# Kernel optimization log

Hardware: AMD Instinct MI355X
Metric: run time of the kernel (lower is better)

The kernel has to match this reference:

```python
import jax, jax.numpy as jnp
import numpy as np

B, D, Q = 1024, 512, 32768


def setup_inputs() -> dict:
    key = jax.random.key(0)
    kx, kq = jax.random.split(key)
    x = jax.random.normal(kx, (B, D), dtype=jnp.float32)
    queue_prev = jax.random.normal(kq, (Q, D), dtype=jnp.float32)
    return {"x": x, "queue_prev": queue_prev}


def reference(x, queue_prev):
    # Queue.forward: enqueue x, keep last queue_size rows (queue assumed full)
    q_size = queue_prev.shape[0]
    queue = jnp.concatenate([queue_prev, x], axis=0)[-q_size:]  # [Q, D]

    # euclidean metric == torch.cdist(x, queue): [B, Q]
    d2 = (
        jnp.sum(x * x, axis=-1, keepdims=True)
        + jnp.sum(queue * queue, axis=-1)[None, :]
        - 2.0 * (x @ queue.T)
    )
    dist = jnp.sqrt(jnp.maximum(d2, 0.0))

    # topk(-dist, 2): two smallest distances; take the 2nd (skip self-match)
    _, indices = jax.lax.top_k(-dist, 2)  # [B, 2]
    nn_idx = indices[:, -1]  # [B]
    return queue[nn_idx]  # [B, D]
```

## Files before the change

kernel.cpp:

```cpp
#include <hip/hip_runtime.h>
#include <hip/hip_bf16.h>
#include <hip/hip_fp16.h>

#define B_N 1024
#define D_N 512
#define Q_N 32768
#define QSHIFT (Q_N - B_N)

#define KP 1024
#define KL 1536
#define BKx 32
#define NKB (KL / BKx)
#define NCH 256

typedef __attribute__((ext_vector_type(8))) _Float16 half8;
typedef __attribute__((ext_vector_type(4))) float f32x4;

__device__ __forceinline__ void top2_update(float d, int j,
                                            float& d1, int& i1, float& d2, int& i2) {
  if (d < d1 || (d == d1 && j < i1)) { d2 = d1; i2 = i1; d1 = d; i1 = j; }
  else if (d < d2 || (d == d2 && j < i2)) { d2 = d; i2 = j; }
}

__global__ __launch_bounds__(256) void prep_kernel(const float* __restrict__ x,
                                                   const float* __restrict__ qp,
                                                   _Float16* __restrict__ Qpk,
                                                   _Float16* __restrict__ Apk,
                                                   float* __restrict__ q2n) {
  const int row  = blockIdx.x * 4 + (threadIdx.x >> 6);
  const int lane = threadIdx.x & 63;
  const bool is_q = row < Q_N;
  const float* src;
  _Float16* dst;
  if (is_q) {
    src = (row < QSHIFT) ? qp + (size_t)(row + B_N) * D_N
                         : x  + (size_t)(row - QSHIFT) * D_N;
    dst = Qpk + (size_t)row * KP;
  } else {
    src = x + (size_t)(row - Q_N) * D_N;
    dst = Apk + (size_t)(row - Q_N) * KP;
  }
  const float4* p = (const float4*)src;
  float4 a = p[lane * 2], b = p[lane * 2 + 1];
  float v[8] = {a.x, a.y, a.z, a.w, b.x, b.y, b.z, b.w};
  _Float16 hi[8] __attribute__((aligned(16)));
  _Float16 lo[8] __attribute__((aligned(16)));
  float s = 0.0f;
  #pragma unroll
  for (int u = 0; u < 8; ++u) {
    s += v[u] * v[u];
    hi[u] = (_Float16)v[u];
    lo[u] = (_Float16)(v[u] - (float)hi[u]);
  }
  *(uint4*)(dst + lane * 8)       = *(const uint4*)hi;
  *(uint4*)(dst + 512 + lane * 8) = *(const uint4*)lo;
  if (is_q) {
    #pragma unroll
    for (int off = 32; off; off >>= 1) s += __shfl_down(s, off);
    if (lane == 0) q2n[row] = s;
  }
}

__global__ __launch_bounds__(256) void nn_mfma(const _Float16* __restrict__ Apk,
                                               const _Float16* __restrict__ Qpk,
                                               const float* __restrict__ q2n,
                                               float4* __restrict__ partial) {
  __shared__ __align__(128) char smem[16384];

  const int chunk = blockIdx.x;
  const int mblk  = blockIdx.y;
  const int n0 = chunk * 128;
  const int i0 = mblk * 128;
  const int t = threadIdx.x;
  const int lane = t & 63;
  const int wv = t >> 6;
  const int wm = (wv >> 1) * 64;
  const int wn = (wv & 1) * 64;
  const int srow = lane >> 2;
  const int scol = (lane & 3) * 8;
  const int fr = lane & 15;
  const int fg = lane >> 4;
  const int fk = fg * 8;

  f32x4 acc[4][4] = {};

  for (int kb = 0; kb < NKB; ++kb) {
    int ka, kq;
    if (kb < 16)      { ka = kb * 32;              kq = kb * 32; }
    else if (kb < 32) { ka = 512 + (kb - 16) * 32; kq = (kb - 16) * 32; }
    else              { ka = (kb - 32) * 32;       kq = 512 + (kb - 32) * 32; }

    __syncthreads();
    #pragma unroll
    for (int c = 0; c < 2; ++c) {
      const int r = c * 64 + wv * 16;
      const _Float16* ga = Apk + (size_t)(i0 + r + srow) * KP + ka + scol;
      const _Float16* gb = Qpk + (size_t)(n0 + r + srow) * KP + kq + scol;
      __builtin_amdgcn_global_load_lds(
          (const __attribute__((address_space(1))) void*)ga,
          (__attribute__((address_space(3))) void*)(smem + r * 64), 16, 0, 0);
      __builtin_amdgcn_global_load_lds(
          (const __attribute__((address_space(1))) void*)gb,
          (__attribute__((address_space(3))) void*)(smem + 8192 + r * 64), 16, 0, 0);
    }
    asm volatile("s_waitcnt vmcnt(0)" ::: "memory");
    __syncthreads();

    half8 af[4], bf[4];
    #pragma unroll
    for (int mi = 0; mi < 4; ++mi)
      af[mi] = *(const half8*)(smem + ((wm + mi * 16 + fr) * 32 + fk) * 2);
    #pragma unroll
    for (int ni = 0; ni < 4; ++ni)
      bf[ni] = *(const half8*)(smem + 8192 + ((wn + ni * 16 + fr) * 32 + fk) * 2);
    #pragma unroll
    for (int mi = 0; mi < 4; ++mi)
      #pragma unroll
      for (int ni = 0; ni < 4; ++ni)
        acc[mi][ni] = __builtin_amdgcn_mfma_f32_16x16x32_f16(af[mi], bf[ni], acc[mi][ni], 0, 0, 0);
  }

  __syncthreads();
  float4 (*red)[8] = (float4(*)[8])smem;

  float q2v[4];
  #pragma unroll
  for (int ni = 0; ni < 4; ++ni) q2v[ni] = q2n[n0 + wn + ni * 16 + fr];

  #pragma unroll
  for (int mi = 0; mi < 4; ++mi) {
    #pragma unroll
    for (int r = 0; r < 4; ++r) {
      float d1 = 3.4e38f, d2v = 3.4e38f;
      int   i1 = 0x7fffffff, i2v = 0x7fffffff;
      #pragma unroll
      for (int ni = 0; ni < 4; ++ni) {
        const float d = q2v[ni] - 2.0f * acc[mi][ni][r];
        top2_update(d, n0 + wn + ni * 16 + fr, d1, i1, d2v, i2v);
      }
      #pragma unroll
      for (int off = 1; off <= 2; off <<= 1) {
        float e1 = __shfl_xor(d1, off);  int j1 = __shfl_xor(i1, off);
        float e2 = __shfl_xor(d2v, off); int j2 = __shfl_xor(i2v, off);
        top2_update(e1, j1, d1, i1, d2v, i2v);
        top2_update(e2, j2, d1, i1, d2v, i2v);
      }
      if ((lane & 3) == 0)
        red[wm + mi * 16 + fg * 4 + r][(wv & 1) * 4 + (fr >> 2)] =
            make_float4(d1, __int_as_float(i1), d2v, __int_as_float(i2v));
    }
  }
  __syncthreads();

  {
    const int row = t >> 1, part = t & 1;
    float d1 = 3.4e38f, d2 = 3.4e38f;
    int   i1 = 0x7fffffff, i2 = 0x7fffffff;
    #pragma unroll
    for (int u = 0; u < 4; ++u) {
      float4 v = red[row][part * 4 + u];
      top2_update(v.x, __float_as_int(v.y), d1, i1, d2, i2);
      top2_update(v.z, __float_as_int(v.w), d1, i1, d2, i2);
    }
    float e1 = __shfl_xor(d1, 1); int j1 = __shfl_xor(i1, 1);
    float e2 = __shfl_xor(d2, 1); int j2 = __shfl_xor(i2, 1);
    top2_update(e1, j1, d1, i1, d2, i2);
    top2_update(e2, j2, d1, i1, d2, i2);
    if (part == 0)
      partial[(size_t)(i0 + row) * NCH + chunk] =
          make_float4(d1, __int_as_float(i1), d2, __int_as_float(i2));
  }
}

__global__ __launch_bounds__(128) void nn_merge256(const float* __restrict__ x,
                                                   const float* __restrict__ qp,
                                                   const float4* __restrict__ partial,
                                                   float* __restrict__ out) {
  const int row = blockIdx.x;
  const int t   = threadIdx.x;
  __shared__ int s_nn;
  if (t < 64) {
    float d1 = 3.4e38f, d2 = 3.4e38f;
    int   i1 = 0x7fffffff, i2 = 0x7fffffff;
    #pragma unroll
    for (int u = 0; u < 4; ++u) {
      float4 v = partial[(size_t)row * NCH + u * 64 + t];
      top2_update(v.x, __float_as_int(v.y), d1, i1, d2, i2);
      top2_update(v.z, __float_as_int(v.w), d1, i1, d2, i2);
    }
    #pragma unroll
    for (int off = 1; off < 64; off <<= 1) {
      float e1 = __shfl_xor(d1, off); int j1 = __shfl_xor(i1, off);
      float e2 = __shfl_xor(d2, off); int j2 = __shfl_xor(i2, off);
      top2_update(e1, j1, d1, i1, d2, i2);
      top2_update(e2, j2, d1, i1, d2, i2);
    }
    if (t == 0) s_nn = i2;
  }
  __syncthreads();
  const int nn = s_nn;
  const float* src = (nn < QSHIFT) ? qp + (size_t)(nn + B_N) * D_N
                                   : x  + (size_t)(nn - QSHIFT) * D_N;
  ((float4*)(out + (size_t)row * D_N))[t] = ((const float4*)src)[t];
}

#define TM 64
#define TN 64
#define BKf 16
#define JCHUNK 512
#define NCHUNK (Q_N / JCHUNK)

__global__ __launch_bounds__(256) void qnorm_kernel(const float* __restrict__ x,
                                                    const float* __restrict__ qp,
                                                    float* __restrict__ q2) {
  const int row  = blockIdx.x * 4 + (threadIdx.x >> 6);
  const int lane = threadIdx.x & 63;
  const float* src = (row < QSHIFT) ? (qp + (size_t)(row + B_N) * D_N)
                                    : (x  + (size_t)(row - QSHIFT) * D_N);
  const float4* p = (const float4*)src;
  float4 a = p[lane];
  float4 b = p[lane + 64];
  float s = a.x*a.x + a.y*a.y + a.z*a.z + a.w*a.w
          + b.x*b.x + b.y*b.y + b.z*b.z + b.w*b.w;
  #pragma unroll
  for (int off = 32; off; off >>= 1) s += __shfl_down(s, off);
  if (lane == 0) q2[row] = s;
}

__global__ __launch_bounds__(256) void nn_main(const float* __restrict__ x,
                                               const float* __restrict__ qp,
                                               const float* __restrict__ q2,
                                               float4* __restrict__ partial) {
  __shared__ float As[BKf][TM];
  __shared__ float Bs[BKf][TN];
  __shared__ float4 red[TM][16];
  const int chunk = blockIdx.x;
  const int i0    = blockIdx.y * TM;
  const int t     = threadIdx.x;
  const int tx    = t & 15;
  const int ty    = t >> 4;
  const int lrow  = t >> 2;
  const int kp    = t & 3;
  float d1[4], d2v[4];
  int   i1[4], i2v[4];
  #pragma unroll
  for (int m = 0; m < 4; ++m) { d1[m] = 3.4e38f; d2v[m] = 3.4e38f; i1[m] = 0x7fffffff; i2v[m] = 0x7fffffff; }
  const int j_base = chunk * JCHUNK;
  for (int jt = 0; jt < JCHUNK / TN; ++jt) {
    const int j0 = j_base + jt * TN;
    float acc[4][4] = {};
    const int jr = j0 + lrow;
    const float* bsrc = (jr < QSHIFT) ? (qp + (size_t)(jr + B_N) * D_N)
                                      : (x  + (size_t)(jr - QSHIFT) * D_N);
    const float* asrc = x + (size_t)(i0 + lrow) * D_N;
    for (int k0 = 0; k0 < D_N; k0 += BKf) {
      float4 a4 = *(const float4*)&asrc[k0 + kp * 4];
      float4 b4 = *(const float4*)&bsrc[k0 + kp * 4];
      __syncthreads();
      As[kp*4+0][lrow] = a4.x; As[kp*4+1][lrow] = a4.y;
      As[kp*4+2][lrow] = a4.z; As[kp*4+3][lrow] = a4.w;
      Bs[kp*4+0][lrow] = b4.x; Bs[kp*4+1][lrow] = b4.y;
      Bs[kp*4+2][lrow] = b4.z; Bs[kp*4+3][lrow] = b4.w;
      __syncthreads();
      #pragma unroll
      for (int kk = 0; kk < BKf; ++kk) {
        float4 av = *(const float4*)&As[kk][ty * 4];
        float4 bv = *(const float4*)&Bs[kk][tx * 4];
        float am[4] = {av.x, av.y, av.z, av.w};
        float bm[4] = {bv.x, bv.y, bv.z, bv.w};
        #pragma unroll
        for (int m = 0; m < 4; ++m)
          #pragma unroll
          for (int c = 0; c < 4; ++c)
            acc[m][c] = fmaf(am[m], bm[c], acc[m][c]);
      }
    }
    #pragma unroll
    for (int m = 0; m < 4; ++m)
      #pragma unroll
      for (int c = 0; c < 4; ++c) {
        const int j = j0 + tx * 4 + c;
        const float d = q2[j] - 2.0f * acc[m][c];
        top2_update(d, j, d1[m], i1[m], d2v[m], i2v[m]);
      }
  }
  __syncthreads();
  #pragma unroll
  for (int m = 0; m < 4; ++m)
    red[ty * 4 + m][tx] = make_float4(d1[m], __int_as_float(i1[m]),
                                      d2v[m], __int_as_float(i2v[m]));
  __syncthreads();
  if (t < TM) {
    float bd1 = 3.4e38f, bd2 = 3.4e38f;
    int   bi1 = 0x7fffffff, bi2 = 0x7fffffff;
    #pragma unroll
    for (int u = 0; u < 16; ++u) {
      float4 v = red[t][u];
      top2_update(v.x, __float_as_int(v.y), bd1, bi1, bd2, bi2);
      top2_update(v.z, __float_as_int(v.w), bd1, bi1, bd2, bi2);
    }
    partial[(size_t)(i0 + t) * NCHUNK + chunk] =
        make_float4(bd1, __int_as_float(bi1), bd2, __int_as_float(bi2));
  }
}

__global__ __launch_bounds__(128) void nn_merge(const float* __restrict__ x,
                                                const float* __restrict__ qp,
                                                const float4* __restrict__ partial,
                                                float* __restrict__ out) {
  const int row = blockIdx.x;
  const int t   = threadIdx.x;
  __shared__ int s_nn;
  if (t < 64) {
    float4 v = partial[(size_t)row * NCHUNK + t];
    float d1 = v.x, d2 = v.z;
    int   i1 = __float_as_int(v.y), i2 = __float_as_int(v.w);
    #pragma unroll
    for (int off = 1; off < 64; off <<= 1) {
      float e1 = __shfl_xor(d1, off); int j1 = __shfl_xor(i1, off);
      float e2 = __shfl_xor(d2, off); int j2 = __shfl_xor(i2, off);
      top2_update(e1, j1, d1, i1, d2, i2);
      top2_update(e2, j2, d1, i1, d2, i2);
    }
    if (t == 0) s_nn = i2;
  }
  __syncthreads();
  const int nn = s_nn;
  const float* src = (nn < QSHIFT) ? (qp + (size_t)(nn + B_N) * D_N)
                                   : (x  + (size_t)(nn - QSHIFT) * D_N);
  *(float4*)&out[(size_t)row * D_N + t * 4] = *(const float4*)&src[t * 4];
}

extern "C" void kernel_launch(void* const* d_in, const int* in_sizes, int n_in,
                              void* d_out, int out_size, void* d_ws, size_t ws_size,
                              hipStream_t stream) {
  const float* x  = (const float*)d_in[0];
  const float* qp = (const float*)d_in[1];
  float* out = (float*)d_out;

  const size_t off_apk = 0;
  const size_t off_qpk = off_apk + (size_t)B_N * KP * sizeof(_Float16);
  const size_t off_q2n = off_qpk + (size_t)Q_N * KP * sizeof(_Float16);
  const size_t off_par = off_q2n + (size_t)Q_N * sizeof(float);
  const size_t need    = off_par + (size_t)B_N * NCH * sizeof(float4);

  if (ws_size >= need) {
    _Float16* Apk = (_Float16*)((char*)d_ws + off_apk);
    _Float16* Qpk = (_Float16*)((char*)d_ws + off_qpk);
    float*    q2n = (float*)((char*)d_ws + off_q2n);
    float4*   par = (float4*)((char*)d_ws + off_par);
    prep_kernel<<<(Q_N + B_N) / 4, 256, 0, stream>>>(x, qp, Qpk, Apk, q2n);
    nn_mfma<<<dim3(NCH, B_N / 128), 256, 0, stream>>>(Apk, Qpk, q2n, par);
    nn_merge256<<<B_N, 128, 0, stream>>>(x, qp, par, out);
  } else {
    float*  q2      = (float*)d_ws;
    float4* partial = (float4*)((char*)d_ws + Q_N * sizeof(float));
    qnorm_kernel<<<Q_N / 4, 256, 0, stream>>>(x, qp, q2);
    nn_main<<<dim3(NCHUNK, B_N / TM), 256, 0, stream>>>(x, qp, q2, partial);
    nn_merge<<<B_N, 128, 0, stream>>>(x, qp, partial, out);
  }
}
```

Measured before the change: 437.7 us.

## Double-buffer LDS tiles, swizzle LDS layout, and remap blocks for locality

```diff
diff --git a/kernel.cpp b/kernel.cpp
--- a/kernel.cpp
+++ b/kernel.cpp
@@ -61,66 +61,79 @@
   }
 }
 
-__global__ __launch_bounds__(256) void nn_mfma(const _Float16* __restrict__ Apk,
-                                               const _Float16* __restrict__ Qpk,
-                                               const float* __restrict__ q2n,
-                                               float4* __restrict__ partial) {
-  __shared__ __align__(128) char smem[16384];
-
-  const int chunk = blockIdx.x;
-  const int mblk  = blockIdx.y;
+__global__ __launch_bounds__(256, 3) void nn_mfma(const _Float16* __restrict__ Apk,
+                                                  const _Float16* __restrict__ Qpk,
+                                                  const float* __restrict__ q2n,
+                                                  float4* __restrict__ partial) {
+  __shared__ __align__(128) char smem[32768];
+
+  const int bid  = blockIdx.x;
+  const int work = (bid & 7) * 256 + (bid >> 3);
+  const int chunk = work >> 3;
+  const int mblk  = work & 7;
   const int n0 = chunk * 128;
   const int i0 = mblk * 128;
+
   const int t = threadIdx.x;
   const int lane = t & 63;
   const int wv = t >> 6;
   const int wm = (wv >> 1) * 64;
   const int wn = (wv & 1) * 64;
   const int srow = lane >> 2;
-  const int scol = (lane & 3) * 8;
+  const int gcol = (((lane & 3) ^ ((lane >> 3) & 3)) * 8);
   const int fr = lane & 15;
   const int fg = lane >> 4;
-  const int fk = fg * 8;
+  const int rswz = (fg ^ ((fr >> 1) & 3)) * 16;
 
   f32x4 acc[4][4] = {};
 
-  for (int kb = 0; kb < NKB; ++kb) {
+  auto stage = [&](int buf, int kb) {
     int ka, kq;
-    if (kb < 16)      { ka = kb * 32;              kq = kb * 32; }
+    if (kb < 16)      { ka = kb * 32;              kq = ka; }
     else if (kb < 32) { ka = 512 + (kb - 16) * 32; kq = (kb - 16) * 32; }
     else              { ka = (kb - 32) * 32;       kq = 512 + (kb - 32) * 32; }
-
-    __syncthreads();
+    char* base = smem + buf * 16384;
     #pragma unroll
     for (int c = 0; c < 2; ++c) {
       const int r = c * 64 + wv * 16;
-      const _Float16* ga = Apk + (size_t)(i0 + r + srow) * KP + ka + scol;
-      const _Float16* gb = Qpk + (size_t)(n0 + r + srow) * KP + kq + scol;
+      const _Float16* ga = Apk + (size_t)(i0 + r + srow) * KP + ka + gcol;
+      const _Float16* gb = Qpk + (size_t)(n0 + r + srow) * KP + kq + gcol;
       __builtin_amdgcn_global_load_lds(
           (const __attribute__((address_space(1))) void*)ga,
-          (__attribute__((address_space(3))) void*)(smem + r * 64), 16, 0, 0);
+          (__attribute__((address_space(3))) void*)(base + r * 64), 16, 0, 0);
       __builtin_amdgcn_global_load_lds(
           (const __attribute__((address_space(1))) void*)gb,
-          (__attribute__((address_space(3))) void*)(smem + 8192 + r * 64), 16, 0, 0);
-    }
+          (__attribute__((address_space(3))) void*)(base + 8192 + r * 64), 16, 0, 0);
+    }
+  };
+
+  stage(0, 0);
+  asm volatile("s_waitcnt vmcnt(0)" ::: "memory");
+  __syncthreads();
+
+  int cur = 0;
+  for (int kb = 0; kb < NKB; ++kb) {
+    if (kb + 1 < NKB) stage(cur ^ 1, kb + 1);
+
+    const char* base = smem + cur * 16384;
+    half8 af[4], bf[4];
+    #pragma unroll
+    for (int mi = 0; mi < 4; ++mi)
+      af[mi] = *(const half8*)(base + (wm + mi * 16 + fr) * 64 + rswz);
+    #pragma unroll
+    for (int ni = 0; ni < 4; ++ni)
+      bf[ni] = *(const half8*)(base + 8192 + (wn + ni * 16 + fr) * 64 + rswz);
+    #pragma unroll
+    for (int mi = 0; mi < 4; ++mi)
+      #pragma unroll
+      for (int ni = 0; ni < 4; ++ni)
+        acc[mi][ni] = __builtin_amdgcn_mfma_f32_16x16x32_f16(af[mi], bf[ni], acc[mi][ni], 0, 0, 0);
+
     asm volatile("s_waitcnt vmcnt(0)" ::: "memory");
     __syncthreads();
-
-    half8 af[4], bf[4];
-    #pragma unroll
-    for (int mi = 0; mi < 4; ++mi)
-      af[mi] = *(const half8*)(smem + ((wm + mi * 16 + fr) * 32 + fk) * 2);
-    #pragma unroll
-    for (int ni = 0; ni < 4; ++ni)
-      bf[ni] = *(const half8*)(smem + 8192 + ((wn + ni * 16 + fr) * 32 + fk) * 2);
-    #pragma unroll
-    for (int mi = 0; mi < 4; ++mi)
-      #pragma unroll
-      for (int ni = 0; ni < 4; ++ni)
-        acc[mi][ni] = __builtin_amdgcn_mfma_f32_16x16x32_f16(af[mi], bf[ni], acc[mi][ni], 0, 0, 0);
-  }
-
-  __syncthreads();
+    cur ^= 1;
+  }
+
   float4 (*red)[8] = (float4(*)[8])smem;
 
   float q2v[4];
@@ -350,7 +363,7 @@
     float*    q2n = (float*)((char*)d_ws + off_q2n);
     float4*   par = (float4*)((char*)d_ws + off_par);
     prep_kernel<<<(Q_N + B_N) / 4, 256, 0, stream>>>(x, qp, Qpk, Apk, q2n);
-    nn_mfma<<<dim3(NCH, B_N / 128), 256, 0, stream>>>(Apk, Qpk, q2n, par);
+    nn_mfma<<<2048, 256, 0, stream>>>(Apk, Qpk, q2n, par);
     nn_merge256<<<B_N, 128, 0, stream>>>(x, qp, par, out);
   } else {
     float*  q2      = (float*)d_ws;
```

Measured after the change: 422.1 us. -3.6%, faster.
